# Kernel optimization log

Hardware: AMD Instinct MI355X
Metric: run time of the kernel (lower is better)

Reference implementation:

```python
import jax, jax.numpy as jnp
import numpy as np

N = 50000   # nodes
D = 128     # input_dim
E = 1600000 # edges
K = 100     # out_nodes


def setup_inputs() -> dict:
    key = jax.random.key(0)
    ks = jax.random.split(key, 9)
    x = jax.random.normal(ks[0], (N, D), dtype=jnp.float32)
    edge_index = jax.random.randint(ks[1], (2, E), 0, N, dtype=jnp.int64)
    # PyG GCNConv params: Linear(in,out,bias=False) weight + separate bias
    s = 1.0 / np.sqrt(D)
    W1 = jax.random.uniform(ks[2], (D, D), jnp.float32, -s, s)
    b1 = jnp.zeros((D,), jnp.float32)
    W2 = jax.random.uniform(ks[3], (D, D), jnp.float32, -s, s)
    b2 = jnp.zeros((D,), jnp.float32)
    Wa = jax.random.uniform(ks[4], (D, K), jnp.float32, -s, s)
    ba = jax.random.uniform(ks[5], (K,), jnp.float32, -s, s)
    return {"x": x, "edge_index": edge_index, "W1": W1, "b1": b1,
            "W2": W2, "b2": b2, "Wa": Wa, "ba": ba}


def _gcn_conv(x, src, dst, norm, W, b, n_nodes):
    # PyG GCNConv: h = x @ W; aggregate D^-1/2 (A+I) D^-1/2 h; add bias
    h = x @ W                                  # [N, D]
    msg = h[src] * norm[:, None]               # [E+N, D] gather + scale
    agg = jax.ops.segment_sum(msg, dst, num_segments=n_nodes)  # scatter-add
    return agg + b


def reference(x, edge_index, W1, b1, W2, b2, Wa, ba):
    n = x.shape[0]
    loop = jnp.arange(n, dtype=edge_index.dtype)
    src = jnp.concatenate([edge_index[0], loop])   # add self-loops
    dst = jnp.concatenate([edge_index[1], loop])
    deg = jnp.zeros((n,), x.dtype).at[dst].add(1.0)
    dinv = jnp.where(deg > 0, jax.lax.rsqrt(deg), 0.0)
    norm = dinv[src] * dinv[dst]                   # [E+N]

    h = _gcn_conv(x, src, dst, norm, W1, b1, n)
    h = jax.nn.relu(h)
    h = _gcn_conv(h, src, dst, norm, W2, b2, n)
    s = jax.nn.softmax(h @ Wa + ba, axis=1)        # [N, K]
    return s
```

## Files before the change

### kernel.cpp

```cpp
#include <hip/hip_runtime.h>

#define D 128
#define KOUT 100
#define CHUNK 4096

typedef __attribute__((ext_vector_type(8))) short short8;
typedef __attribute__((ext_vector_type(4))) float floatx4;

__device__ inline float bf_lo(unsigned int u) { return __uint_as_float(u << 16); }
__device__ inline float bf_hi(unsigned int u) { return __uint_as_float(u & 0xFFFF0000u); }

__device__ inline unsigned int bf_round(float a) {
    unsigned int ua = __float_as_uint(a);
    return (ua + 0x7FFFu + ((ua >> 16) & 1u)) >> 16;
}
__device__ inline unsigned int pack_bf(float a, float b) {
    return bf_round(a) | (bf_round(b) << 16);
}

__device__ void gemm_body(const void* __restrict__ Xin, const unsigned short* __restrict__ Wf,
                          const float* __restrict__ bias,
                          void* __restrict__ Y, int nrows, int in_bf16, int out_mode,
                          float* lds_f, int tile) {
    unsigned short* lds_h = (unsigned short*)lds_f;
    unsigned int* lds_u = (unsigned int*)lds_f;

    int tid = threadIdx.x;
    int w = tid >> 6, lane = tid & 63;
    int quad = lane >> 4, m16 = lane & 15;
    int r0 = tile * 64;

    if (!in_bf16) {
        int row = tid >> 2, cg_ = tid & 3;
        bool valid = (r0 + row) < nrows;
        const float4* Xr = (const float4*)Xin + (size_t)(r0 + row) * 32 + cg_ * 8;
#pragma unroll
        for (int j = 0; j < 8; j++) {
            float4 v = valid ? Xr[j] : make_float4(0.f, 0.f, 0.f, 0.f);
            int c = cg_ * 32 + j * 4;
            lds_u[row * 68 + (c >> 1)]     = pack_bf(v.x, v.y);
            lds_u[row * 68 + (c >> 1) + 1] = pack_bf(v.z, v.w);
        }
        __syncthreads();
    }

    floatx4 acc[8];
#pragma unroll
    for (int ct = 0; ct < 8; ct++) acc[ct] = (floatx4){0.f, 0.f, 0.f, 0.f};

    int arow = r0 + w * 16 + m16;
    if (arow > nrows - 1) arow = nrows - 1;
    const unsigned int* Xb = (const unsigned int*)Xin;

    const short8* Wf8 = (const short8*)Wf;
#pragma unroll
    for (int kt = 0; kt < 4; kt++) {
        short8 a;
        if (in_bf16) {
            a = *(const short8*)(Xb + (size_t)arow * 64 + kt * 16 + quad * 4);
        } else {
            a = *(const short8*)(lds_h + (w * 16 + m16) * 136 + kt * 32 + quad * 8);
        }
#pragma unroll
        for (int ct = 0; ct < 8; ct++) {
            short8 b = Wf8[(kt * 8 + ct) * 64 + lane];
            acc[ct] = __builtin_amdgcn_mfma_f32_16x16x32_bf16(a, b, acc[ct], 0, 0, 0);
        }
    }

    if (out_mode == 1) {
        __syncthreads();
#pragma unroll
        for (int ct = 0; ct < 8; ct++) {
#pragma unroll
            for (int r = 0; r < 4; r++) {
                int rl = w * 16 + quad * 4 + r;
                lds_f[rl * 130 + ct * 16 + m16] = acc[ct][r];
            }
        }
        __syncthreads();
        unsigned int* Yb = (unsigned int*)Y;
        for (int r = 0; r < 16; r++) {
            int row = r0 + w * 16 + r;
            if (row < nrows) {
                float lo = lds_f[(w * 16 + r) * 130 + 2 * lane];
                float hi = lds_f[(w * 16 + r) * 130 + 2 * lane + 1];
                Yb[(size_t)row * 64 + lane] = pack_bf(lo, hi);
            }
        }
    } else {
        float bb[8];
#pragma unroll
        for (int ct = 0; ct < 8; ct++) bb[ct] = bias[ct * 16 + m16];
        float* Yf = (float*)Y;
#pragma unroll
        for (int r = 0; r < 4; r++) {
            int row = r0 + w * 16 + quad * 4 + r;
            float vv[8];
            float mx = -1e30f;
#pragma unroll
            for (int ct = 0; ct < 8; ct++) {
                int col = ct * 16 + m16;
                vv[ct] = (col < KOUT) ? acc[ct][r] + bb[ct] : -1e30f;
                mx = fmaxf(mx, vv[ct]);
            }
#pragma unroll
            for (int off = 1; off < 16; off <<= 1) mx = fmaxf(mx, __shfl_xor(mx, off));
            float se = 0.f;
#pragma unroll
            for (int ct = 0; ct < 8; ct++) {
                vv[ct] = (vv[ct] > -1e29f) ? __expf(vv[ct] - mx) : 0.f;
                se += vv[ct];
            }
#pragma unroll
            for (int off = 1; off < 16; off <<= 1) se += __shfl_xor(se, off);
            float inv = 1.f / se;
            if (row < nrows) {
#pragma unroll
                for (int ct = 0; ct < 8; ct++) {
                    int col = ct * 16 + m16;
                    if (col < KOUT) Yf[(size_t)row * KOUT + col] = vv[ct] * inv;
                }
            }
        }
    }
}


__launch_bounds__(256)
__global__ void k_p1_prep(const int* __restrict__ ei, int E, int nbuck, int cap,
                          int* __restrict__ bcur, unsigned int* __restrict__ bdata,
                          const float* __restrict__ W1, const float* __restrict__ W2,
                          const float* __restrict__ Wa, const float* __restrict__ ba,
                          const float* __restrict__ b2,
                          unsigned short* __restrict__ Wf1, unsigned short* __restrict__ WfF,
                          float* __restrict__ bpad, int* __restrict__ rowptr,
                          float* __restrict__ dinv,
                          unsigned int* __restrict__ zrowA, unsigned int* __restrict__ zrowB,
                          int n, int nbP1) {
    __shared__ float lds_f[64 * 130];
    int tid = threadIdx.x;

    if ((int)blockIdx.x < nbP1) {
        int* hist = (int*)lds_f;
        int* sc   = hist + 256;
        int* pfx  = sc + 256;
        int* cur  = pfx + 256;
        int* gbase = cur + 256;
        unsigned int* lbuf = (unsigned int*)(gbase + 256);
        unsigned char* bkt = (unsigned char*)(lbuf + CHUNK);

        int base = blockIdx.x * CHUNK;
        int cnt = E - base; if (cnt > CHUNK) cnt = CHUNK;

        hist[tid] = 0;
        __syncthreads();

        int src[CHUNK / 256];
        int dst[CHUNK / 256];
#pragma unroll
        for (int q = 0; q < CHUNK / 256; q++) {
            int li = tid + q * 256;
            if (li < cnt) {
                src[q] = ei[base + li];
                dst[q] = ei[E + base + li];
                atomicAdd(&hist[dst[q] >> 8], 1);
            }
        }
        __syncthreads();

        int v = hist[tid];
        sc[tid] = v;
        __syncthreads();
        for (int off = 1; off < 256; off <<= 1) {
            int t = (tid >= off) ? sc[tid - off] : 0;
            __syncthreads();
            sc[tid] += t;
            __syncthreads();
        }
        int excl = sc[tid] - v;
        pfx[tid] = excl;
        cur[tid] = excl;
        gbase[tid] = 0;
        if (tid < nbuck && v > 0) gbase[tid] = atomicAdd(&bcur[tid], v);
        __syncthreads();

#pragma unroll
        for (int q = 0; q < CHUNK / 256; q++) {
            int li = tid + q * 256;
            if (li < cnt) {
                int b = dst[q] >> 8;
                int p = atomicAdd(&cur[b], 1);
                lbuf[p] = (unsigned int)src[q] | ((unsigned int)(dst[q] & 255) << 24);
                bkt[p] = (unsigned char)b;
            }
        }
        __syncthreads();

        for (int p = tid; p < cnt; p += 256) {
            int b = bkt[p];
            bdata[(size_t)b * cap + gbase[b] + (p - pfx[b])] = lbuf[p];
        }
    } else {
        int idx = ((int)blockIdx.x - nbP1) * 256 + tid;
        if (idx < 2 * 16384) {
            int m = idx >> 14;
            int e = idx & 16383;
            int j = e & 7, lane = (e >> 3) & 63, ct = (e >> 9) & 7, kt = e >> 12;
            int k = kt * 32 + (lane >> 4) * 8 + j;
            int col = ct * 16 + (lane & 15);
            if (m == 0) {
                Wf1[e] = (unsigned short)bf_round(W1[k * 128 + col]);
            } else {
                float s = 0.f;
                if (col < KOUT) {
                    const float* w2r = W2 + k * 128;
#pragma unroll 8
                    for (int mm = 0; mm < 128; mm++)
                        s = fmaf(w2r[mm], Wa[mm * KOUT + col], s);
                }
                WfF[e] = (unsigned short)bf_round(s);
            }
        }
        if (idx < 128) {
            float s = 0.f;
            if (idx < KOUT) {
                for (int mm = 0; mm < 128; mm++)
                    s = fmaf(b2[mm], Wa[mm * KOUT + idx], s);
                s += ba[idx];
            }
            bpad[idx] = s;
        }
        if (idx < 64) { zrowA[idx] = 0u; zrowB[idx] = 0u; }
        if (idx == 64) rowptr[n] = E;
        if (idx == 65) dinv[n] = 0.f;
    }
}


__launch_bounds__(256)
__global__ void k_build_gemm(const unsigned int* __restrict__ bdata, const int* __restrict__ bcur,
                             int cap, float* __restrict__ dinv,
                             int* __restrict__ rowptr, int* __restrict__ csr,
                             int n, int nbuck,
                             const float* __restrict__ X, const unsigned short* __restrict__ Wf1,
                             unsigned int* __restrict__ HbA) {
    __shared__ float lds_f[64 * 130];
    int tid = threadIdx.x;

    if ((int)blockIdx.x < nbuck) {
        int* cnts = (int*)lds_f;
        int* sc   = cnts + 256;
        int* cur  = sc + 256;
        int* pbb  = cur + 256;

        int b = blockIdx.x;
        if (tid == 0) pbb[0] = 0;
        cnts[tid] = 0;
        __syncthreads();

        int part = 0;
        for (int t = tid; t < b; t += 256) part += bcur[t];
#pragma unroll
        for (int off = 32; off > 0; off >>= 1) part += __shfl_down(part, off);
        if ((tid & 63) == 0 && part != 0) atomicAdd(&pbb[0], part);

        int cnt = bcur[b];
        const unsigned int* p = bdata + (size_t)b * cap;
        for (int e = tid; e < cnt; e += 256) atomicAdd(&cnts[p[e] >> 24], 1);
        __syncthreads();

        int v = cnts[tid];
        sc[tid] = v;
        __syncthreads();
        for (int off = 1; off < 256; off <<= 1) {
            int t = (tid >= off) ? sc[tid - off] : 0;
            __syncthreads();
            sc[tid] += t;
            __syncthreads();
        }
        int gstart = pbb[0] + (sc[tid] - v);
        int node = b * 256 + tid;
        if (node < n) {
            dinv[node] = rsqrtf((float)(v + 1));
            rowptr[node] = gstart;
        }
        cur[tid] = gstart;
        __syncthreads();

        for (int e = tid; e < cnt; e += 256) {
            unsigned int u = p[e];
            int pos = atomicAdd(&cur[u >> 24], 1);
            csr[pos] = (int)(u & 0xFFFFFFu);
        }
    } else {
        gemm_body(X, Wf1, nullptr, HbA, n, 0, 1, lds_f, (int)blockIdx.x - nbuck);
    }
}

__launch_bounds__(256)
__global__ void k_gemm_final(const void* __restrict__ Xin, const unsigned short* __restrict__ WfF,
                             const float* __restrict__ bpad, void* __restrict__ out, int n) {
    __shared__ float lds_f[64 * 130];
    gemm_body(Xin, WfF, bpad, out, n, 1, 2, lds_f, (int)blockIdx.x);
}


__launch_bounds__(256)
__global__ void agg_gather_kernel(const uint4* __restrict__ Hb4, const int* __restrict__ csr,
                                  const int* __restrict__ rowptr, const float* __restrict__ dinv,
                                  const float* __restrict__ bias,
                                  unsigned int* __restrict__ Ob, int n) {
    int wid = threadIdx.x >> 6, lane = threadIdx.x & 63;
    int g = lane >> 4, c = lane & 15;
    int i = blockIdx.x * 4 + wid;
    if (i >= n) return;

    int start = rowptr[i];
    int cnt = rowptr[i + 1] - start;
    const int* cp = csr + start;
    float di = rsqrtf((float)(cnt + 1));

    float acc[8];
    {
        uint4 sv = Hb4[(size_t)i * 16 + c];
        unsigned int su[4] = {sv.x, sv.y, sv.z, sv.w};
        if (g != 0) { su[0] = su[1] = su[2] = su[3] = 0u; }
#pragma unroll
        for (int t = 0; t < 4; t++) {
            acc[2 * t]     = di * bf_lo(su[t]);
            acc[2 * t + 1] = di * bf_hi(su[t]);
        }
    }

    int s[4];
    float dv[4];
#pragma unroll
    for (int u = 0; u < 4; u++) {
        int idx = u * 4 + g;
        s[u] = (idx < cnt) ? cp[idx] : n;
    }
#pragma unroll
    for (int u = 0; u < 4; u++) dv[u] = dinv[s[u]];

    for (int e = 0; e < cnt; e += 16) {
        uint4 v[4];
#pragma unroll
        for (int u = 0; u < 4; u++) v[u] = Hb4[(size_t)s[u] * 16 + c];
        int ns[4];
#pragma unroll
        for (int u = 0; u < 4; u++) {
            int idx = e + 16 + u * 4 + g;
            ns[u] = (idx < cnt) ? cp[idx] : n;
        }
        float ndv[4];
#pragma unroll
        for (int u = 0; u < 4; u++) ndv[u] = dinv[ns[u]];
#pragma unroll
        for (int u = 0; u < 4; u++) {
            unsigned int uu[4] = {v[u].x, v[u].y, v[u].z, v[u].w};
#pragma unroll
            for (int t = 0; t < 4; t++) {
                acc[2 * t]     = fmaf(dv[u], bf_lo(uu[t]), acc[2 * t]);
                acc[2 * t + 1] = fmaf(dv[u], bf_hi(uu[t]), acc[2 * t + 1]);
            }
        }
#pragma unroll
        for (int u = 0; u < 4; u++) { s[u] = ns[u]; dv[u] = ndv[u]; }
    }

#pragma unroll
    for (int j = 0; j < 8; j++) {
        acc[j] += __shfl_xor(acc[j], 16);
        acc[j] += __shfl_xor(acc[j], 32);
    }

    float2 bb = ((const float2*)bias)[c * 4 + g];
    float fx = acc[g * 2]     * di + bb.x;
    float fy = acc[g * 2 + 1] * di + bb.y;
    fx = fmaxf(fx, 0.f); fy = fmaxf(fy, 0.f);
    fx *= di; fy *= di;
    Ob[(size_t)i * 64 + c * 4 + g] = pack_bf(fx, fy);
}


__launch_bounds__(256)
__global__ void agg_pre_kernel(const uint4* __restrict__ Hb4, const int* __restrict__ csr,
                               const int* __restrict__ rowptr,
                               unsigned int* __restrict__ Ob, int n) {
    int wid = threadIdx.x >> 6, lane = threadIdx.x & 63;
    int g = lane >> 4, c = lane & 15;
    int i = blockIdx.x * 4 + wid;
    if (i >= n) return;

    int start = rowptr[i];
    int cnt = rowptr[i + 1] - start;
    const int* cp = csr + start;
    float di = rsqrtf((float)(cnt + 1));

    float acc[8];
    {
        uint4 sv = Hb4[(size_t)i * 16 + c];
        unsigned int su[4] = {sv.x, sv.y, sv.z, sv.w};
        if (g != 0) { su[0] = su[1] = su[2] = su[3] = 0u; }
#pragma unroll
        for (int t = 0; t < 4; t++) {
            acc[2 * t]     = bf_lo(su[t]);
            acc[2 * t + 1] = bf_hi(su[t]);
        }
    }

    int s[4];
#pragma unroll
    for (int u = 0; u < 4; u++) {
        int idx = u * 4 + g;
        s[u] = (idx < cnt) ? cp[idx] : n;
    }
    for (int e = 0; e < cnt; e += 16) {
        uint4 v[4];
#pragma unroll
        for (int u = 0; u < 4; u++) v[u] = Hb4[(size_t)s[u] * 16 + c];
        int ns[4];
#pragma unroll
        for (int u = 0; u < 4; u++) {
            int idx = e + 16 + u * 4 + g;
            ns[u] = (idx < cnt) ? cp[idx] : n;
        }
#pragma unroll
        for (int u = 0; u < 4; u++) {
            unsigned int uu[4] = {v[u].x, v[u].y, v[u].z, v[u].w};
#pragma unroll
            for (int t = 0; t < 4; t++) {
                acc[2 * t]     += bf_lo(uu[t]);
                acc[2 * t + 1] += bf_hi(uu[t]);
            }
        }
#pragma unroll
        for (int u = 0; u < 4; u++) s[u] = ns[u];
    }

#pragma unroll
    for (int j = 0; j < 8; j++) {
        acc[j] += __shfl_xor(acc[j], 16);
        acc[j] += __shfl_xor(acc[j], 32);
    }

    float fx = acc[g * 2]     * di;
    float fy = acc[g * 2 + 1] * di;
    Ob[(size_t)i * 64 + c * 4 + g] = pack_bf(fx, fy);
}


extern "C" void kernel_launch(void* const* d_in, const int* in_sizes, int n_in,
                              void* d_out, int out_size, void* d_ws, size_t ws_size,
                              hipStream_t stream) {
    const float* x  = (const float*)d_in[0];
    const int*   ei = (const int*)d_in[1];
    const float* W1 = (const float*)d_in[2];
    const float* b1 = (const float*)d_in[3];
    const float* W2 = (const float*)d_in[4];
    const float* b2 = (const float*)d_in[5];
    const float* Wa = (const float*)d_in[6];
    const float* ba = (const float*)d_in[7];
    float* out = (float*)d_out;

    int N = in_sizes[0] / D;
    int E = in_sizes[1] / 2;

    int nbuck = (N + 255) >> 8;
    int cap = ((E / nbuck) + 2048 + 63) & ~63;

    char* w = (char*)d_ws;
    size_t off = 0;
    auto carve = [&](size_t bytes) -> void* {
        void* p = w + off;
        off = (off + bytes + 255) & ~(size_t)255;
        return p;
    };
    int*   bcur   = (int*)carve(256 * 4);
    float* dinv   = (float*)carve((size_t)(N + 1) * 4);
    int*   rowptr = (int*)carve((size_t)(N + 1) * 4);
    unsigned int* bdata = (unsigned int*)carve((size_t)nbuck * cap * 4);
    int*   csr    = (int*)carve((size_t)E * 4);
    unsigned short* Wf1 = (unsigned short*)carve(16384 * 2);
    unsigned short* WfF = (unsigned short*)carve(16384 * 2);
    float* bpad   = (float*)carve(512);
    unsigned int* HbA = (unsigned int*)carve((size_t)(N + 1) * 64 * 4);
    unsigned int* HbB = (unsigned int*)carve((size_t)(N + 1) * 64 * 4);
    (void)ws_size; (void)n_in; (void)out_size;

    int nbNode4 = (N + 3) / 4;
    int nbGemm = (N + 63) / 64;
    int nbP1 = (E + CHUNK - 1) / CHUNK;

    (void)hipMemsetAsync(bcur, 0, 256 * 4, stream);

    k_p1_prep<<<nbP1 + 128, 256, 0, stream>>>(ei, E, nbuck, cap, bcur, bdata,
                                              W1, W2, Wa, ba, b2, Wf1, WfF, bpad,
                                              rowptr, dinv,
                                              HbA + (size_t)N * 64, HbB + (size_t)N * 64,
                                              N, nbP1);
    k_build_gemm<<<nbuck + nbGemm, 256, 0, stream>>>(bdata, bcur, cap, dinv, rowptr, csr,
                                                     N, nbuck, x, Wf1, HbA);
    agg_gather_kernel<<<nbNode4, 256, 0, stream>>>((const uint4*)HbA, csr, rowptr, dinv, b1, HbB, N);
    agg_pre_kernel<<<nbNode4, 256, 0, stream>>>((const uint4*)HbB, csr, rowptr, HbA, N);
    k_gemm_final<<<nbGemm, 256, 0, stream>>>(HbA, WfF, bpad, out, N);
}
```

Measured before the change: 237.4 us.

## Fuse second aggregation with final GEMM and softmax into one kernel

Merges the second-layer gather aggregation with the fused (W2·Wa) GEMM and softmax. Each 512-thread block aggregates 64 nodes into LDS as bf16, then runs the MFMA GEMM and a split-column softmax with cross-wave reductions through shared memory. This removes one kernel launch and the bf16 intermediate write and read of the aggregated features. In exchange each wave aggregates 8 nodes one after another, and the GEMM phase waits on the slowest wave in the block, which can lower gather parallelism and latency hiding.

Result: slower. 247.7 us (+4.3%).

```diff
diff --git a/kernel.cpp b/kernel.cpp
--- a/kernel.cpp
+++ b/kernel.cpp
@@ -19,9 +19,7 @@
 }
 
 __device__ void gemm_body(const void* __restrict__ Xin, const unsigned short* __restrict__ Wf,
-                          const float* __restrict__ bias,
-                          void* __restrict__ Y, int nrows, int in_bf16, int out_mode,
-                          float* lds_f, int tile) {
+                          void* __restrict__ Y, int nrows, float* lds_f, int tile) {
     unsigned short* lds_h = (unsigned short*)lds_f;
     unsigned int* lds_u = (unsigned int*)lds_f;
 
@@ -30,7 +28,7 @@
     int quad = lane >> 4, m16 = lane & 15;
     int r0 = tile * 64;
 
-    if (!in_bf16) {
+    {
         int row = tid >> 2, cg_ = tid & 3;
         bool valid = (r0 + row) < nrows;
         const float4* Xr = (const float4*)Xin + (size_t)(r0 + row) * 32 + cg_ * 8;
@@ -48,19 +46,10 @@
 #pragma unroll
     for (int ct = 0; ct < 8; ct++) acc[ct] = (floatx4){0.f, 0.f, 0.f, 0.f};
 
-    int arow = r0 + w * 16 + m16;
-    if (arow > nrows - 1) arow = nrows - 1;
-    const unsigned int* Xb = (const unsigned int*)Xin;
-
     const short8* Wf8 = (const short8*)Wf;
 #pragma unroll
     for (int kt = 0; kt < 4; kt++) {
-        short8 a;
-        if (in_bf16) {
-            a = *(const short8*)(Xb + (size_t)arow * 64 + kt * 16 + quad * 4);
-        } else {
-            a = *(const short8*)(lds_h + (w * 16 + m16) * 136 + kt * 32 + quad * 8);
-        }
+        short8 a = *(const short8*)(lds_h + (w * 16 + m16) * 136 + kt * 32 + quad * 8);
 #pragma unroll
         for (int ct = 0; ct < 8; ct++) {
             short8 b = Wf8[(kt * 8 + ct) * 64 + lane];
@@ -68,60 +57,23 @@
         }
     }
 
-    if (out_mode == 1) {
-        __syncthreads();
-#pragma unroll
-        for (int ct = 0; ct < 8; ct++) {
-#pragma unroll
-            for (int r = 0; r < 4; r++) {
-                int rl = w * 16 + quad * 4 + r;
-                lds_f[rl * 130 + ct * 16 + m16] = acc[ct][r];
-            }
-        }
-        __syncthreads();
-        unsigned int* Yb = (unsigned int*)Y;
-        for (int r = 0; r < 16; r++) {
-            int row = r0 + w * 16 + r;
-            if (row < nrows) {
-                float lo = lds_f[(w * 16 + r) * 130 + 2 * lane];
-                float hi = lds_f[(w * 16 + r) * 130 + 2 * lane + 1];
-                Yb[(size_t)row * 64 + lane] = pack_bf(lo, hi);
-            }
-        }
-    } else {
-        float bb[8];
-#pragma unroll
-        for (int ct = 0; ct < 8; ct++) bb[ct] = bias[ct * 16 + m16];
-        float* Yf = (float*)Y;
+    __syncthreads();
+#pragma unroll
+    for (int ct = 0; ct < 8; ct++) {
 #pragma unroll
         for (int r = 0; r < 4; r++) {
-            int row = r0 + w * 16 + quad * 4 + r;
-            float vv[8];
-            float mx = -1e30f;
-#pragma unroll
-            for (int ct = 0; ct < 8; ct++) {
-                int col = ct * 16 + m16;
-                vv[ct] = (col < KOUT) ? acc[ct][r] + bb[ct] : -1e30f;
-                mx = fmaxf(mx, vv[ct]);
-            }
-#pragma unroll
-            for (int off = 1; off < 16; off <<= 1) mx = fmaxf(mx, __shfl_xor(mx, off));
-            float se = 0.f;
-#pragma unroll
-            for (int ct = 0; ct < 8; ct++) {
-                vv[ct] = (vv[ct] > -1e29f) ? __expf(vv[ct] - mx) : 0.f;
-                se += vv[ct];
-            }
-#pragma unroll
-            for (int off = 1; off < 16; off <<= 1) se += __shfl_xor(se, off);
-            float inv = 1.f / se;
-            if (row < nrows) {
-#pragma unroll
-                for (int ct = 0; ct < 8; ct++) {
-                    int col = ct * 16 + m16;
-                    if (col < KOUT) Yf[(size_t)row * KOUT + col] = vv[ct] * inv;
-                }
-            }
+            int rl = w * 16 + quad * 4 + r;
+            lds_f[rl * 130 + ct * 16 + m16] = acc[ct][r];
+        }
+    }
+    __syncthreads();
+    unsigned int* Yb = (unsigned int*)Y;
+    for (int r = 0; r < 16; r++) {
+        int row = r0 + w * 16 + r;
+        if (row < nrows) {
+            float lo = lds_f[(w * 16 + r) * 130 + 2 * lane];
+            float hi = lds_f[(w * 16 + r) * 130 + 2 * lane + 1];
+            Yb[(size_t)row * 64 + lane] = pack_bf(lo, hi);
         }
     }
 }
@@ -294,15 +246,8 @@
             csr[pos] = (int)(u & 0xFFFFFFu);
         }
     } else {
-        gemm_body(X, Wf1, nullptr, HbA, n, 0, 1, lds_f, (int)blockIdx.x - nbuck);
-    }
-}
-
-__launch_bounds__(256)
-__global__ void k_gemm_final(const void* __restrict__ Xin, const unsigned short* __restrict__ WfF,
-                             const float* __restrict__ bpad, void* __restrict__ out, int n) {
-    __shared__ float lds_f[64 * 130];
-    gemm_body(Xin, WfF, bpad, out, n, 1, 2, lds_f, (int)blockIdx.x);
+        gemm_body(X, Wf1, HbA, n, lds_f, (int)blockIdx.x - nbuck);
+    }
 }
 
 
@@ -384,70 +329,155 @@
 }
 
 
-__launch_bounds__(256)
-__global__ void agg_pre_kernel(const uint4* __restrict__ Hb4, const int* __restrict__ csr,
-                               const int* __restrict__ rowptr,
-                               unsigned int* __restrict__ Ob, int n) {
-    int wid = threadIdx.x >> 6, lane = threadIdx.x & 63;
-    int g = lane >> 4, c = lane & 15;
-    int i = blockIdx.x * 4 + wid;
-    if (i >= n) return;
-
-    int start = rowptr[i];
-    int cnt = rowptr[i + 1] - start;
-    const int* cp = csr + start;
-    float di = rsqrtf((float)(cnt + 1));
-
-    float acc[8];
+__launch_bounds__(512)
+__global__ void k_agg2_gemm(const uint4* __restrict__ Hb4, const int* __restrict__ csr,
+                            const int* __restrict__ rowptr,
+                            const unsigned short* __restrict__ WfF,
+                            const float* __restrict__ bpad,
+                            float* __restrict__ out, int n) {
+    __shared__ unsigned int lds_u[64 * 68];
+    __shared__ float sred_mx[2][64];
+    __shared__ float sred_se[2][64];
+
+    int tid = threadIdx.x;
+    int wid = tid >> 6, lane = tid & 63;
+    int r0 = blockIdx.x * 64;
+
     {
-        uint4 sv = Hb4[(size_t)i * 16 + c];
-        unsigned int su[4] = {sv.x, sv.y, sv.z, sv.w};
-        if (g != 0) { su[0] = su[1] = su[2] = su[3] = 0u; }
-#pragma unroll
-        for (int t = 0; t < 4; t++) {
-            acc[2 * t]     = bf_lo(su[t]);
-            acc[2 * t + 1] = bf_hi(su[t]);
-        }
-    }
-
-    int s[4];
-#pragma unroll
-    for (int u = 0; u < 4; u++) {
-        int idx = u * 4 + g;
-        s[u] = (idx < cnt) ? cp[idx] : n;
-    }
-    for (int e = 0; e < cnt; e += 16) {
-        uint4 v[4];
-#pragma unroll
-        for (int u = 0; u < 4; u++) v[u] = Hb4[(size_t)s[u] * 16 + c];
-        int ns[4];
-#pragma unroll
-        for (int u = 0; u < 4; u++) {
-            int idx = e + 16 + u * 4 + g;
-            ns[u] = (idx < cnt) ? cp[idx] : n;
-        }
-#pragma unroll
-        for (int u = 0; u < 4; u++) {
-            unsigned int uu[4] = {v[u].x, v[u].y, v[u].z, v[u].w};
-#pragma unroll
-            for (int t = 0; t < 4; t++) {
-                acc[2 * t]     += bf_lo(uu[t]);
-                acc[2 * t + 1] += bf_hi(uu[t]);
-            }
-        }
-#pragma unroll
-        for (int u = 0; u < 4; u++) s[u] = ns[u];
-    }
-
-#pragma unroll
-    for (int j = 0; j < 8; j++) {
-        acc[j] += __shfl_xor(acc[j], 16);
-        acc[j] += __shfl_xor(acc[j], 32);
-    }
-
-    float fx = acc[g * 2]     * di;
-    float fy = acc[g * 2 + 1] * di;
-    Ob[(size_t)i * 64 + c * 4 + g] = pack_bf(fx, fy);
+        int g = lane >> 4, c = lane & 15;
+        for (int it = 0; it < 8; it++) {
+            int lrow = wid * 8 + it;
+            int i = r0 + lrow;
+            bool alive = i < n;
+            int node = alive ? i : n;
+            int start = 0, cnt = 0;
+            if (alive) { start = rowptr[i]; cnt = rowptr[i + 1] - start; }
+            const int* cp = csr + start;
+            float di = rsqrtf((float)(cnt + 1));
+
+            float acc[8];
+            {
+                uint4 sv = Hb4[(size_t)node * 16 + c];
+                unsigned int su[4] = {sv.x, sv.y, sv.z, sv.w};
+                if (g != 0) { su[0] = su[1] = su[2] = su[3] = 0u; }
+#pragma unroll
+                for (int t = 0; t < 4; t++) {
+                    acc[2 * t]     = bf_lo(su[t]);
+                    acc[2 * t + 1] = bf_hi(su[t]);
+                }
+            }
+
+            int s[4];
+#pragma unroll
+            for (int u = 0; u < 4; u++) {
+                int idx = u * 4 + g;
+                s[u] = (idx < cnt) ? cp[idx] : n;
+            }
+            for (int e = 0; e < cnt; e += 16) {
+                uint4 v[4];
+#pragma unroll
+                for (int u = 0; u < 4; u++) v[u] = Hb4[(size_t)s[u] * 16 + c];
+                int ns[4];
+#pragma unroll
+                for (int u = 0; u < 4; u++) {
+                    int idx = e + 16 + u * 4 + g;
+                    ns[u] = (idx < cnt) ? cp[idx] : n;
+                }
+#pragma unroll
+                for (int u = 0; u < 4; u++) {
+                    unsigned int uu[4] = {v[u].x, v[u].y, v[u].z, v[u].w};
+#pragma unroll
+                    for (int t = 0; t < 4; t++) {
+                        acc[2 * t]     += bf_lo(uu[t]);
+                        acc[2 * t + 1] += bf_hi(uu[t]);
+                    }
+                }
+#pragma unroll
+                for (int u = 0; u < 4; u++) s[u] = ns[u];
+            }
+
+#pragma unroll
+            for (int j = 0; j < 8; j++) {
+                acc[j] += __shfl_xor(acc[j], 16);
+                acc[j] += __shfl_xor(acc[j], 32);
+            }
+
+            lds_u[lrow * 68 + c * 4 + g] = pack_bf(acc[g * 2] * di, acc[g * 2 + 1] * di);
+        }
+    }
+    __syncthreads();
+
+    int w4 = wid & 3, h = wid >> 2;
+    int quad = lane >> 4, m16 = lane & 15;
+    const unsigned short* lds_h = (const unsigned short*)lds_u;
+
+    floatx4 acc[4];
+#pragma unroll
+    for (int ctl = 0; ctl < 4; ctl++) acc[ctl] = (floatx4){0.f, 0.f, 0.f, 0.f};
+
+    const short8* Wf8 = (const short8*)WfF;
+#pragma unroll
+    for (int kt = 0; kt < 4; kt++) {
+        short8 a = *(const short8*)(lds_h + (w4 * 16 + m16) * 136 + kt * 32 + quad * 8);
+#pragma unroll
+        for (int ctl = 0; ctl < 4; ctl++) {
+            int ct = h * 4 + ctl;
+            short8 b = Wf8[(kt * 8 + ct) * 64 + lane];
+            acc[ctl] = __builtin_amdgcn_mfma_f32_16x16x32_bf16(a, b, acc[ctl], 0, 0, 0);
+        }
+    }
+
+    float bb[4];
+#pragma unroll
+    for (int ctl = 0; ctl < 4; ctl++) bb[ctl] = bpad[(h * 4 + ctl) * 16 + m16];
+
+    float vvA[4][4];
+#pragma unroll
+    for (int r = 0; r < 4; r++) {
+        int lrow = w4 * 16 + quad * 4 + r;
+        float mx = -1e30f;
+#pragma unroll
+        for (int ctl = 0; ctl < 4; ctl++) {
+            int col = (h * 4 + ctl) * 16 + m16;
+            vvA[r][ctl] = (col < KOUT) ? acc[ctl][r] + bb[ctl] : -1e30f;
+            mx = fmaxf(mx, vvA[r][ctl]);
+        }
+#pragma unroll
+        for (int off = 1; off < 16; off <<= 1) mx = fmaxf(mx, __shfl_xor(mx, off));
+        if (m16 == 0) sred_mx[h][lrow] = mx;
+    }
+    __syncthreads();
+
+#pragma unroll
+    for (int r = 0; r < 4; r++) {
+        int lrow = w4 * 16 + quad * 4 + r;
+        float mx = fmaxf(sred_mx[0][lrow], sred_mx[1][lrow]);
+        float se = 0.f;
+#pragma unroll
+        for (int ctl = 0; ctl < 4; ctl++) {
+            float v = (vvA[r][ctl] > -1e29f) ? __expf(vvA[r][ctl] - mx) : 0.f;
+            vvA[r][ctl] = v;
+            se += v;
+        }
+#pragma unroll
+        for (int off = 1; off < 16; off <<= 1) se += __shfl_xor(se, off);
+        if (m16 == 0) sred_se[h][lrow] = se;
+    }
+    __syncthreads();
+
+#pragma unroll
+    for (int r = 0; r < 4; r++) {
+        int lrow = w4 * 16 + quad * 4 + r;
+        int row = r0 + lrow;
+        float inv = 1.f / (sred_se[0][lrow] + sred_se[1][lrow]);
+        if (row < n) {
+#pragma unroll
+            for (int ctl = 0; ctl < 4; ctl++) {
+                int col = (h * 4 + ctl) * 16 + m16;
+                if (col < KOUT) out[(size_t)row * KOUT + col] = vvA[r][ctl] * inv;
+            }
+        }
+    }
 }
 
 
@@ -503,6 +533,5 @@
     k_build_gemm<<<nbuck + nbGemm, 256, 0, stream>>>(bdata, bcur, cap, dinv, rowptr, csr,
                                                      N, nbuck, x, Wf1, HbA);
     agg_gather_kernel<<<nbNode4, 256, 0, stream>>>((const uint4*)HbA, csr, rowptr, dinv, b1, HbB, N);
-    agg_pre_kernel<<<nbNode4, 256, 0, stream>>>((const uint4*)HbB, csr, rowptr, HbA, N);
-    k_gemm_final<<<nbGemm, 256, 0, stream>>>(HbA, WfF, bpad, out, N);
-}
+    k_agg2_gemm<<<nbGemm, 512, 0, stream>>>((const uint4*)HbB, csr, rowptr, WfF, bpad, out, N);
+}
```
